# Performance work log

Measured on AMD Instinct MI355X. Metric: run time of the kernel, lower is better.

## Reference

```python
import jax, jax.numpy as jnp
import numpy as np

NUM_HEADS = 16
NEG_BIG = -1.0e9


def setup_inputs() -> dict:
    key = jax.random.key(0)
    k1, k2, k3 = jax.random.split(key, 3)
    B, S, D = 2, 2048, 1024
    x = jax.random.normal(k1, (B, S, D), dtype=jnp.float32)
    qkv_weights = jax.random.normal(k2, (D, 3 * D), dtype=jnp.float32) * (1.0 / np.sqrt(D))
    output_weights = jax.random.normal(k3, (D, D), dtype=jnp.float32) * (1.0 / np.sqrt(D))
    return {"x": x, "qkv_weights": qkv_weights, "output_weights": output_weights}


def reference(x, qkv_weights, output_weights):
    B, S, D = x.shape
    H = NUM_HEADS
    hd = D // H
    qkv = jnp.einsum('bsd,de->bse', x, qkv_weights)  # [B,S,3D]
    q, k, v = jnp.split(qkv, 3, axis=-1)
    # [B,H,S,hd]
    q = q.reshape(B, S, H, hd).transpose(0, 2, 1, 3)
    k = k.reshape(B, S, H, hd).transpose(0, 2, 1, 3)
    v = v.reshape(B, S, H, hd).transpose(0, 2, 1, 3)
    scores = jnp.einsum('bhqd,bhkd->bhqk', q, k)  # unscaled, matches original masked path
    # original bug: when masked, softmax is applied to UNSCALED scores with mask
    tril = jnp.tril(jnp.ones((S, S), dtype=scores.dtype))
    masked = scores * tril + NEG_BIG * (1.0 - tril)
    attn = jax.nn.softmax(masked, axis=-1)
    heads = jnp.einsum('bhqk,bhkd->bhqd', attn, v)  # [B,H,S,hd]
    merged = heads.transpose(0, 2, 1, 3).reshape(B, S, D)
    return jnp.einsum('bsd,de->bse', merged, output_weights)
```

## Files before the change

kernel.cpp:

```cpp
#include <hip/hip_runtime.h>
#include <stdint.h>

using u16 = unsigned short;
typedef __attribute__((ext_vector_type(8))) _Float16 half8;
typedef __attribute__((ext_vector_type(4))) float f32x4;
typedef __attribute__((ext_vector_type(4))) unsigned short u16x4;

#define S_LEN 2048
#define D_MODEL 1024
#define NHEAD 16
#define HDIM 64

__device__ __forceinline__ u16 f2h_bits(float f){
    _Float16 h = (_Float16)f;
    return __builtin_bit_cast(u16, h);
}
__device__ __forceinline__ float h2f_bits(u16 v){
    return (float)__builtin_bit_cast(_Float16, v);
}

typedef __attribute__((address_space(1))) void gvoid;
typedef __attribute__((address_space(3))) void lvoid;
__device__ __forceinline__ void gload_lds16(const u16* g, u16* l){
    __builtin_amdgcn_global_load_lds((gvoid*)(uintptr_t)g, (lvoid*)l, 16, 0, 0);
}

__device__ __constant__ signed char QB_T[40] = {3,7,7,10,11,11,11,14,14,15,15,15,15, 6,6,9,9,10,10,12,12,13,13,13,13,14,14, 2,5,5,8,8,8,9,12,12, 4,4, 1, 0};
__device__ __constant__ signed char LO_T[40] = {0,0,8,0,0,8,16,0,8,0,8,16,24, 0,7,0,7,8,15,0,7,0,7,14,21,16,23, 0,0,6,0,6,12,14,14,20, 0,5, 0, 0};
__device__ __constant__ signed char HI_T[40] = {8,8,16,8,8,16,24,8,16,8,16,24,32, 7,14,7,14,15,22,7,14,7,14,21,28,23,30, 6,6,12,6,12,18,20,20,26, 5,10, 4, 2};
__device__ __constant__ signed char PO_T[40] = {-1,6,7,14,17,18,19,28,29,32,33,34,35, 4,5,11,12,15,16,20,21,24,25,26,27,30,31, -1,2,3,8,9,10,13,22,23, 0,1, -1, -1};
__device__ __constant__ signed char NP_T[12] = {2,2,2,2,3,3,3,3,4,4,4,4};
__device__ __constant__ signed char OF_T[12] = {0,2,4,6,8,11,14,17,20,24,28,32};

__global__ __launch_bounds__(256) void k_cvt_x(const float* __restrict__ x, u16* __restrict__ xh){
    int i = blockIdx.x*256 + threadIdx.x;
    float4 v = reinterpret_cast<const float4*>(x)[i];
    u16x4 o;
    o.x = f2h_bits(v.x); o.y = f2h_bits(v.y); o.z = f2h_bits(v.z); o.w = f2h_bits(v.w);
    reinterpret_cast<u16x4*>(xh)[i] = o;
}

__global__ __launch_bounds__(256) void k_cvt_w(const float* __restrict__ W0, u16* __restrict__ T0,
                                               const float* __restrict__ W1, u16* __restrict__ T1){
    __shared__ float tt[32][33];
    int bx = blockIdx.x;
    const float* W; u16* WT; int N, n0;
    if (bx < 96){ W = W0; WT = T0; N = 3072; n0 = bx*32; }
    else        { W = W1; WT = T1; N = 1024; n0 = (bx-96)*32; }
    int k0 = blockIdx.y*32;
    int tx = threadIdx.x & 31, ty = threadIdx.x >> 5;
    #pragma unroll
    for (int i=0;i<4;++i) tt[ty+8*i][tx] = W[(size_t)(k0+ty+8*i)*N + n0+tx];
    __syncthreads();
    #pragma unroll
    for (int i=0;i<4;++i) WT[(size_t)(n0+ty+8*i)*1024 + k0+tx] = f2h_bits(tt[tx][ty+8*i]);
}

template<int EPI>
__global__ __launch_bounds__(256) void k_gemm(const u16* __restrict__ A, const u16* __restrict__ BT,
                                              float* __restrict__ Cf, u16* __restrict__ Qh,
                                              u16* __restrict__ Kh, u16* __restrict__ Vt){
    constexpr int Kd = 1024;
    __shared__ u16 As[2*128*32];
    __shared__ u16 Bs[2*128*32];
    int nwg = gridDim.x;
    int cpx = nwg >> 3;
    int wg  = ((int)blockIdx.x & 7)*cpx + ((int)blockIdx.x >> 3);
    int tm = wg & 31, tn = wg >> 5;
    int t = threadIdx.x;
    int w = t >> 6, lane = t & 63;
    int lr = lane & 15, lg = lane >> 4;
    int wm = (w>>1)*64, wn = (w&1)*64;
    int m0 = tm*128 + wm, n0 = tn*128 + wn;

    const u16* aG = A  + (size_t)(tm*128 + (t>>2))*Kd + (t&3)*8;
    const u16* bG = BT + (size_t)(tn*128 + (t>>2))*Kd + (t&3)*8;
    u16* aL = As + (t>>2)*32 + (t&3)*8;
    u16* bL = Bs + (t>>2)*32 + (t&3)*8;

    auto stage = [&](int buf, int kk){
        gload_lds16(aG + kk, aL + buf*4096);
        gload_lds16(aG + kk + (size_t)64*Kd, aL + buf*4096 + 64*32);
        gload_lds16(bG + kk, bL + buf*4096);
        gload_lds16(bG + kk + (size_t)64*Kd, bL + buf*4096 + 64*32);
    };

    f32x4 acc[4][4];
    #pragma unroll
    for (int i=0;i<4;++i)
        #pragma unroll
        for (int j=0;j<4;++j) acc[i][j] = (f32x4){0.f,0.f,0.f,0.f};

    stage(0, 0);
    __syncthreads();
    for (int kk=0; kk<Kd; kk+=32){
        int cur = (kk>>5) & 1;
        if (kk+32 < Kd) stage(cur^1, kk+32);

        half8 av[4], bv[4];
        #pragma unroll
        for (int mf=0;mf<4;++mf) av[mf] = *reinterpret_cast<const half8*>(&As[cur*4096 + (wm+mf*16+lr)*32 + lg*8]);
        #pragma unroll
        for (int nf=0;nf<4;++nf) bv[nf] = *reinterpret_cast<const half8*>(&Bs[cur*4096 + (wn+nf*16+lr)*32 + lg*8]);
        __builtin_amdgcn_s_setprio(1);
        #pragma unroll
        for (int mf=0;mf<4;++mf)
            #pragma unroll
            for (int nf=0;nf<4;++nf)
                acc[mf][nf] = __builtin_amdgcn_mfma_f32_16x16x32_f16(av[mf], bv[nf], acc[mf][nf], 0,0,0);
        __builtin_amdgcn_s_setprio(0);
        __syncthreads();
    }

    if (EPI == 0){
        #pragma unroll
        for (int mf=0;mf<4;++mf)
            #pragma unroll
            for (int nf=0;nf<4;++nf)
                #pragma unroll
                for (int j=0;j<4;++j)
                    Cf[(size_t)(m0+mf*16+lg*4+j)*D_MODEL + n0+nf*16+lr] = acc[mf][nf][j];
    } else {
        #pragma unroll
        for (int mf=0;mf<4;++mf){
            int r0 = m0 + mf*16 + lg*4;
            int b  = r0 >> 11, s = r0 & 2047;
            #pragma unroll
            for (int nf=0;nf<4;++nf){
                int col = n0 + nf*16 + lr;
                int which = col >> 10;
                int d  = col & 1023;
                int h  = d >> 6, di = d & 63;
                int bh = b*NHEAD + h;
                if (which == 2){
                    u16x4 pv;
                    pv.x = f2h_bits(acc[mf][nf][0]);
                    pv.y = f2h_bits(acc[mf][nf][1]);
                    pv.z = f2h_bits(acc[mf][nf][2]);
                    pv.w = f2h_bits(acc[mf][nf][3]);
                    *reinterpret_cast<u16x4*>(Vt + ((size_t)bh*HDIM + di)*S_LEN + s) = pv;
                } else {
                    u16* dst = (which==0 ? Qh : Kh) + ((size_t)bh*S_LEN + s)*HDIM + di;
                    #pragma unroll
                    for (int j=0;j<4;++j) dst[(size_t)j*HDIM] = f2h_bits(acc[mf][nf][j]);
                }
            }
        }
    }
}

__global__ __launch_bounds__(256,3) void k_attn(const u16* __restrict__ Q, const u16* __restrict__ K,
                                                const u16* __restrict__ Vt, u16* __restrict__ Mg,
                                                u16* __restrict__ On, float* __restrict__ Ml,
                                                float* __restrict__ Ll){
    __shared__ u16 Kl[2*64*64];
    __shared__ u16 Vl[2*64*64];
    __shared__ u16 plds[4][32][72];
    int t = threadIdx.x;
    int w = t >> 6, lane = t & 63;
    int lr = lane & 15, lg = lane >> 4;
    int blk = blockIdx.x;
    int bh  = blk & 31;
    int pi  = blk >> 5;
    int qb   = QB_T[pi];
    int ktLo = LO_T[pi];
    int ktHi = HI_T[pi];
    int po   = PO_T[pi];
    bool split = (po >= 0);
    int q0w = qb*128 + w*32;
    int b = bh >> 4, h = bh & 15;
    int pid = split ? bh*36 + po : 0;
    const u16* Qp = Q  + (size_t)bh*S_LEN*HDIM;
    const u16* Kp = K  + (size_t)bh*S_LEN*HDIM;
    const u16* Vp = Vt + (size_t)bh*HDIM*S_LEN;

    int c0 = t, c1 = t + 256;
    int r0 = c0 >> 3, s0 = 8*((c0 & 7) ^ (r0 & 7));
    int r1 = c1 >> 3, s1 = 8*((c1 & 7) ^ (r1 & 7));
    const u16* Ks0 = Kp + (size_t)r0*HDIM + s0;
    const u16* Ks1 = Kp + (size_t)r1*HDIM + s1;
    const u16* Vs0 = Vp + (size_t)r0*S_LEN + s0;
    const u16* Vs1 = Vp + (size_t)r1*S_LEN + s1;
    u16* Kd0 = Kl + c0*8; u16* Kd1 = Kl + c1*8;
    u16* Vd0 = Vl + c0*8; u16* Vd1 = Vl + c1*8;

    auto stageKV = [&](int buf, int kt){
        int kbase = kt*64;
        gload_lds16(Ks0 + (size_t)kbase*HDIM, Kd0 + buf*4096);
        gload_lds16(Ks1 + (size_t)kbase*HDIM, Kd1 + buf*4096);
        gload_lds16(Vs0 + kbase, Vd0 + buf*4096);
        gload_lds16(Vs1 + kbase, Vd1 + buf*4096);
    };

    half8 qf[2][2];
    #pragma unroll
    for (int qi=0;qi<2;++qi)
        #pragma unroll
        for (int ks=0;ks<2;++ks){
            half8 v = *reinterpret_cast<const half8*>(Qp + (size_t)(q0w+qi*16+lr)*HDIM + ks*32 + lg*8);
            #pragma unroll
            for (int j=0;j<8;++j) v[j] = v[j] * (_Float16)1.44269504f;
            qf[qi][ks] = v;
        }

    f32x4 oacc[2][4];
    float mrow[2], lrow[2];
    #pragma unroll
    for (int mf=0;mf<2;++mf){
        #pragma unroll
        for (int nf=0;nf<4;++nf) oacc[mf][nf] = (f32x4){0.f,0.f,0.f,0.f};
        mrow[mf] = -1e30f; lrow[mf] = 0.f;
    }

    int lastkt = (q0w + 31) >> 6;
    int swz = (lr & 7)*8;
    int nT = ktHi - ktLo;

    stageKV(0, ktLo);
    __syncthreads();
    for (int i=0; i<nT; ++i){
        int kt = ktLo + i;
        int cur = i & 1;
        if (i+1 < nT) stageKV(cur^1, kt+1);

        if (kt <= lastkt){
            const u16* Kb = Kl + cur*4096;
            const u16* Vb = Vl + cur*4096;
            int kbase = kt*64;
            half8 kfr[4][2];
            #pragma unroll
            for (int kf=0;kf<4;++kf)
                #pragma unroll
                for (int ks=0;ks<2;++ks)
                    kfr[kf][ks] = *reinterpret_cast<const half8*>(Kb + (kf*16+lr)*64 + ((ks*32 + lg*8) ^ swz));
            f32x4 sc[4][2];
            #pragma unroll
            for (int kf=0;kf<4;++kf)
                #pragma unroll
                for (int qi=0;qi<2;++qi) sc[kf][qi] = (f32x4){0.f,0.f,0.f,0.f};
            __builtin_amdgcn_s_setprio(1);
            #pragma unroll
            for (int kf=0;kf<4;++kf)
                #pragma unroll
                for (int qi=0;qi<2;++qi)
                    #pragma unroll
                    for (int ks=0;ks<2;++ks)
                        sc[kf][qi] = __builtin_amdgcn_mfma_f32_16x16x32_f16(kfr[kf][ks], qf[qi][ks], sc[kf][qi], 0,0,0);
            __builtin_amdgcn_s_setprio(0);

            half8 vf[4][2];
            #pragma unroll
            for (int nf=0;nf<4;++nf)
                #pragma unroll
                for (int kh=0;kh<2;++kh)
                    vf[nf][kh] = *reinterpret_cast<const half8*>(Vb + (nf*16+lr)*64 + ((kh*32 + lg*8) ^ swz));

            if (kt == lastkt){
                #pragma unroll
                for (int kf=0;kf<4;++kf)
                    #pragma unroll
                    for (int qi=0;qi<2;++qi)
                        #pragma unroll
                        for (int j=0;j<4;++j)
                            if (kbase+kf*16+lg*4+j > q0w+qi*16+lr) sc[kf][qi][j] = -1e9f;
            }

            float pmax[2];
            #pragma unroll
            for (int qi=0;qi<2;++qi){
                float t0 = fmaxf(fmaxf(sc[0][qi][0], sc[0][qi][1]), fmaxf(sc[0][qi][2], sc[0][qi][3]));
                float t1 = fmaxf(fmaxf(sc[1][qi][0], sc[1][qi][1]), fmaxf(sc[1][qi][2], sc[1][qi][3]));
                float t2 = fmaxf(fmaxf(sc[2][qi][0], sc[2][qi][1]), fmaxf(sc[2][qi][2], sc[2][qi][3]));
                float t3 = fmaxf(fmaxf(sc[3][qi][0], sc[3][qi][1]), fmaxf(sc[3][qi][2], sc[3][qi][3]));
                float tm = fmaxf(fmaxf(t0,t1), fmaxf(t2,t3));
                tm = fmaxf(tm, __shfl_xor(tm,16));
                tm = fmaxf(tm, __shfl_xor(tm,32));
                pmax[qi] = tm;
            }
            bool need = (pmax[0] > mrow[0]+8.0f) || (pmax[1] > mrow[1]+8.0f);
            if (__any(need)){
                float aq[2];
                #pragma unroll
                for (int qi=0;qi<2;++qi){
                    float mnew = fmaxf(mrow[qi], pmax[qi]);
                    aq[qi] = __builtin_amdgcn_exp2f(mrow[qi] - mnew);
                    mrow[qi] = mnew;
                    lrow[qi] *= aq[qi];
                }
                float am[2][4];
                #pragma unroll
                for (int mf=0;mf<2;++mf)
                    #pragma unroll
                    for (int j=0;j<4;++j) am[mf][j] = __shfl(aq[mf], lg*4+j);
                #pragma unroll
                for (int mf=0;mf<2;++mf)
                    #pragma unroll
                    for (int nf=0;nf<4;++nf)
                        #pragma unroll
                        for (int j=0;j<4;++j) oacc[mf][nf][j] *= am[mf][j];
            }
            #pragma unroll
            for (int qi=0;qi<2;++qi){
                float m = mrow[qi];
                float rs = 0.f;
                #pragma unroll
                for (int kf=0;kf<4;++kf)
                    #pragma unroll
                    for (int j=0;j<4;++j){
                        float e = __builtin_amdgcn_exp2f(sc[kf][qi][j] - m);
                        sc[kf][qi][j] = e;
                        rs += e;
                    }
                rs += __shfl_xor(rs,16);
                rs += __shfl_xor(rs,32);
                lrow[qi] += rs;
            }
            #pragma unroll
            for (int kf=0;kf<4;++kf)
                #pragma unroll
                for (int qi=0;qi<2;++qi){
                    u16x4 pk;
                    pk.x = f2h_bits(sc[kf][qi][0]);
                    pk.y = f2h_bits(sc[kf][qi][1]);
                    pk.z = f2h_bits(sc[kf][qi][2]);
                    pk.w = f2h_bits(sc[kf][qi][3]);
                    *reinterpret_cast<u16x4*>(&plds[w][qi*16+lr][kf*16+lg*4]) = pk;
                }
            half8 pa[2][2];
            #pragma unroll
            for (int mf=0;mf<2;++mf)
                #pragma unroll
                for (int kh=0;kh<2;++kh)
                    pa[mf][kh] = *reinterpret_cast<const half8*>(&plds[w][mf*16+lr][kh*32 + lg*8]);
            __builtin_amdgcn_s_setprio(1);
            #pragma unroll
            for (int mf=0;mf<2;++mf)
                #pragma unroll
                for (int nf=0;nf<4;++nf)
                    #pragma unroll
                    for (int kh=0;kh<2;++kh)
                        oacc[mf][nf] = __builtin_amdgcn_mfma_f32_16x16x32_f16(pa[mf][kh], vf[nf][kh], oacc[mf][nf], 0,0,0);
            __builtin_amdgcn_s_setprio(0);
        }
        __syncthreads();
    }

    float linv[2][4];
    #pragma unroll
    for (int mf=0;mf<2;++mf)
        #pragma unroll
        for (int j=0;j<4;++j) linv[mf][j] = 1.0f/__shfl(lrow[mf], lg*4+j);
    if (!split){
        #pragma unroll
        for (int mf=0;mf<2;++mf)
            #pragma unroll
            for (int nf=0;nf<4;++nf)
                #pragma unroll
                for (int j=0;j<4;++j)
                    Mg[(size_t)(b*S_LEN + q0w + mf*16 + lg*4 + j)*D_MODEL + h*HDIM + nf*16 + lr]
                        = f2h_bits(oacc[mf][nf][j]*linv[mf][j]);
    } else {
        #pragma unroll
        for (int mf=0;mf<2;++mf)
            #pragma unroll
            for (int nf=0;nf<4;++nf)
                #pragma unroll
                for (int j=0;j<4;++j)
                    On[(size_t)pid*8192 + (w*32 + mf*16 + lg*4 + j)*64 + nf*16 + lr]
                        = f2h_bits(oacc[mf][nf][j]*linv[mf][j]);
        if (lg == 0){
            #pragma unroll
            for (int qi=0;qi<2;++qi){
                Ml[pid*128 + w*32 + qi*16 + lr] = mrow[qi];
                Ll[pid*128 + w*32 + qi*16 + lr] = lrow[qi];
            }
        }
    }
}

__global__ __launch_bounds__(256) void k_comb(const u16* __restrict__ On, const float* __restrict__ Ml,
                                              const float* __restrict__ Ll, u16* __restrict__ Mg){
    int blk = blockIdx.x;
    int bh = blk & 31;
    int rest = blk >> 5;
    int qi = rest >> 3;
    int rq = rest & 7;
    int qb = 4 + qi;
    int np = NP_T[qi];
    int base = bh*36 + OF_T[qi];
    int b = bh >> 4, h = bh & 15;
    int t = threadIdx.x;
    int r  = rq*16 + (t >> 4);
    int cc = (t & 15) * 4;
    float osum0=0.f, osum1=0.f, osum2=0.f, osum3=0.f, wsum=0.f;
    float mm[4], ll[4];
    float M = -1e30f;
    #pragma unroll
    for (int p=0;p<4;++p){
        if (p < np){
            mm[p] = Ml[(base+p)*128 + r];
            ll[p] = Ll[(base+p)*128 + r];
            M = fmaxf(M, mm[p]);
        }
    }
    #pragma unroll
    for (int p=0;p<4;++p){
        if (p < np){
            float wgt = ll[p]*__builtin_amdgcn_exp2f(mm[p] - M);
            u16x4 ov = *reinterpret_cast<const u16x4*>(On + (size_t)(base+p)*8192 + r*64 + cc);
            osum0 += wgt*h2f_bits(ov[0]);
            osum1 += wgt*h2f_bits(ov[1]);
            osum2 += wgt*h2f_bits(ov[2]);
            osum3 += wgt*h2f_bits(ov[3]);
            wsum  += wgt;
        }
    }
    float inv = 1.0f/wsum;
    u16x4 o;
    o[0] = f2h_bits(osum0*inv);
    o[1] = f2h_bits(osum1*inv);
    o[2] = f2h_bits(osum2*inv);
    o[3] = f2h_bits(osum3*inv);
    *reinterpret_cast<u16x4*>(Mg + (size_t)(b*S_LEN + qb*128 + r)*D_MODEL + h*HDIM + cc) = o;
}

extern "C" void kernel_launch(void* const* d_in, const int* in_sizes, int n_in,
                              void* d_out, int out_size, void* d_ws, size_t ws_size,
                              hipStream_t stream) {
    const float* x    = (const float*)d_in[0];
    const float* wqkv = (const float*)d_in[1];
    const float* wout = (const float*)d_in[2];
    float* out = (float*)d_out;
    char* ws = (char*)d_ws;

    const size_t MB = 1u<<20;
    u16* xh     = (u16*)(ws + 0*MB);
    u16* wqkvT  = (u16*)(ws + 8*MB);
    u16* woutT  = (u16*)(ws + 14*MB);
    u16* Qh     = (u16*)(ws + 16*MB);
    u16* Kh     = (u16*)(ws + 24*MB);
    u16* Vt     = (u16*)(ws + 32*MB);
    u16* Mg     = (u16*)(ws + 40*MB);
    u16* On     = (u16*)(ws + 48*MB);
    float* Ml   = (float*)(ws + 67*MB);
    float* Ll   = (float*)(ws + 67*MB + 640*1024);

    k_cvt_x <<<4096, 256, 0, stream>>>(x, xh);
    k_cvt_w <<<dim3(128,32), 256, 0, stream>>>(wqkv, wqkvT, wout, woutT);
    k_gemm<1><<<768, 256, 0, stream>>>(xh, wqkvT, nullptr, Qh, Kh, Vt);
    k_attn  <<<1280, 256, 0, stream>>>(Qh, Kh, Vt, Mg, On, Ml, Ll);
    k_comb  <<<3072, 256, 0, stream>>>(On, Ml, Ll, Mg);
    k_gemm<0><<<256, 256, 0, stream>>>(Mg, woutT, out, nullptr, nullptr, nullptr);
}
```

Baseline: 118.2 us.

## Enlarge attention query tile to 256 rows with 8 waves and fuse conversion kernels

The attention kernel now processes 256 query rows per block with 512 threads (8 waves), so each staged K/V tile in LDS is shared by twice as many waves. The causal work-split tables, partial-output layout and combine kernel indexing are rebuilt for the coarser blocks. The x and weight conversion kernels are merged into a single launch. This removes one launch and halves K/V staging traffic per query row, but the coarser tiles give the causal schedule less load-balancing granularity and the larger blocks may lower occupancy.

```diff
diff --git a/kernel.cpp b/kernel.cpp
--- a/kernel.cpp
+++ b/kernel.cpp
@@ -25,29 +25,32 @@
     __builtin_amdgcn_global_load_lds((gvoid*)(uintptr_t)g, (lvoid*)l, 16, 0, 0);
 }
 
-__device__ __constant__ signed char QB_T[40] = {3,7,7,10,11,11,11,14,14,15,15,15,15, 6,6,9,9,10,10,12,12,13,13,13,13,14,14, 2,5,5,8,8,8,9,12,12, 4,4, 1, 0};
-__device__ __constant__ signed char LO_T[40] = {0,0,8,0,0,8,16,0,8,0,8,16,24, 0,7,0,7,8,15,0,7,0,7,14,21,16,23, 0,0,6,0,6,12,14,14,20, 0,5, 0, 0};
-__device__ __constant__ signed char HI_T[40] = {8,8,16,8,8,16,24,8,16,8,16,24,32, 7,14,7,14,15,22,7,14,7,14,21,28,23,30, 6,6,12,6,12,18,20,20,26, 5,10, 4, 2};
-__device__ __constant__ signed char PO_T[40] = {-1,6,7,14,17,18,19,28,29,32,33,34,35, 4,5,11,12,15,16,20,21,24,25,26,27,30,31, -1,2,3,8,9,10,13,22,23, 0,1, -1, -1};
-__device__ __constant__ signed char NP_T[12] = {2,2,2,2,3,3,3,3,4,4,4,4};
-__device__ __constant__ signed char OF_T[12] = {0,2,4,6,8,11,14,17,20,24,28,32};
-
-__global__ __launch_bounds__(256) void k_cvt_x(const float* __restrict__ x, u16* __restrict__ xh){
-    int i = blockIdx.x*256 + threadIdx.x;
-    float4 v = reinterpret_cast<const float4*>(x)[i];
-    u16x4 o;
-    o.x = f2h_bits(v.x); o.y = f2h_bits(v.y); o.z = f2h_bits(v.z); o.w = f2h_bits(v.w);
-    reinterpret_cast<u16x4*>(xh)[i] = o;
-}
-
-__global__ __launch_bounds__(256) void k_cvt_w(const float* __restrict__ W0, u16* __restrict__ T0,
-                                               const float* __restrict__ W1, u16* __restrict__ T1){
+__device__ __constant__ signed char QB_T[20] = {1,3,3,5,5,5,7,7,7,7, 4,4,6,6,6,6, 2,2,4, 0};
+__device__ __constant__ signed char LO_T[20] = {0,0,8,0,8,16,0,8,16,24, 0,7,0,7,14,21, 0,6,14, 0};
+__device__ __constant__ signed char HI_T[20] = {8,8,16,8,16,24,8,16,24,32, 7,14,7,14,21,28, 6,12,20, 4};
+__device__ __constant__ signed char PO_T[20] = {-1,2,3,7,8,9,14,15,16,17, 4,5,10,11,12,13, 0,1,6, -1};
+__device__ __constant__ signed char NP_T[6] = {2,2,3,3,4,4};
+__device__ __constant__ signed char OF_T[6] = {0,2,4,7,10,14};
+
+__global__ __launch_bounds__(256) void k_cvt(const float* __restrict__ x, u16* __restrict__ xh,
+                                             const float* __restrict__ W0, u16* __restrict__ T0,
+                                             const float* __restrict__ W1, u16* __restrict__ T1){
     __shared__ float tt[32][33];
-    int bx = blockIdx.x;
+    int blk = blockIdx.x;
+    if (blk < 4096){
+        int i = blk*256 + threadIdx.x;
+        float4 v = reinterpret_cast<const float4*>(x)[i];
+        u16x4 o;
+        o.x = f2h_bits(v.x); o.y = f2h_bits(v.y); o.z = f2h_bits(v.z); o.w = f2h_bits(v.w);
+        reinterpret_cast<u16x4*>(xh)[i] = o;
+        return;
+    }
+    int wi = blk - 4096;
+    int bx = wi & 127, ky = wi >> 7;
     const float* W; u16* WT; int N, n0;
     if (bx < 96){ W = W0; WT = T0; N = 3072; n0 = bx*32; }
     else        { W = W1; WT = T1; N = 1024; n0 = (bx-96)*32; }
-    int k0 = blockIdx.y*32;
+    int k0 = ky*32;
     int tx = threadIdx.x & 31, ty = threadIdx.x >> 5;
     #pragma unroll
     for (int i=0;i<4;++i) tt[ty+8*i][tx] = W[(size_t)(k0+ty+8*i)*N + n0+tx];
@@ -149,13 +152,13 @@
     }
 }
 
-__global__ __launch_bounds__(256,3) void k_attn(const u16* __restrict__ Q, const u16* __restrict__ K,
-                                                const u16* __restrict__ Vt, u16* __restrict__ Mg,
-                                                u16* __restrict__ On, float* __restrict__ Ml,
-                                                float* __restrict__ Ll){
+__global__ __launch_bounds__(512) void k_attn(const u16* __restrict__ Q, const u16* __restrict__ K,
+                                              const u16* __restrict__ Vt, u16* __restrict__ Mg,
+                                              u16* __restrict__ On, float* __restrict__ Ml,
+                                              float* __restrict__ Ll){
     __shared__ u16 Kl[2*64*64];
     __shared__ u16 Vl[2*64*64];
-    __shared__ u16 plds[4][32][72];
+    __shared__ u16 plds[8][32][72];
     int t = threadIdx.x;
     int w = t >> 6, lane = t & 63;
     int lr = lane & 15, lg = lane >> 4;
@@ -167,29 +170,23 @@
     int ktHi = HI_T[pi];
     int po   = PO_T[pi];
     bool split = (po >= 0);
-    int q0w = qb*128 + w*32;
+    int q0w = qb*256 + w*32;
     int b = bh >> 4, h = bh & 15;
-    int pid = split ? bh*36 + po : 0;
+    int pid = split ? bh*18 + po : 0;
     const u16* Qp = Q  + (size_t)bh*S_LEN*HDIM;
     const u16* Kp = K  + (size_t)bh*S_LEN*HDIM;
     const u16* Vp = Vt + (size_t)bh*HDIM*S_LEN;
 
-    int c0 = t, c1 = t + 256;
-    int r0 = c0 >> 3, s0 = 8*((c0 & 7) ^ (r0 & 7));
-    int r1 = c1 >> 3, s1 = 8*((c1 & 7) ^ (r1 & 7));
-    const u16* Ks0 = Kp + (size_t)r0*HDIM + s0;
-    const u16* Ks1 = Kp + (size_t)r1*HDIM + s1;
-    const u16* Vs0 = Vp + (size_t)r0*S_LEN + s0;
-    const u16* Vs1 = Vp + (size_t)r1*S_LEN + s1;
-    u16* Kd0 = Kl + c0*8; u16* Kd1 = Kl + c1*8;
-    u16* Vd0 = Vl + c0*8; u16* Vd1 = Vl + c1*8;
+    int r0 = t >> 3, s0 = 8*((t & 7) ^ (r0 & 7));
+    const u16* Ks = Kp + (size_t)r0*HDIM + s0;
+    const u16* Vs = Vp + (size_t)r0*S_LEN + s0;
+    u16* Kd = Kl + t*8;
+    u16* Vd = Vl + t*8;
 
     auto stageKV = [&](int buf, int kt){
         int kbase = kt*64;
-        gload_lds16(Ks0 + (size_t)kbase*HDIM, Kd0 + buf*4096);
-        gload_lds16(Ks1 + (size_t)kbase*HDIM, Kd1 + buf*4096);
-        gload_lds16(Vs0 + kbase, Vd0 + buf*4096);
-        gload_lds16(Vs1 + kbase, Vd1 + buf*4096);
+        gload_lds16(Ks + (size_t)kbase*HDIM, Kd + buf*4096);
+        gload_lds16(Vs + kbase, Vd + buf*4096);
     };
 
     half8 qf[2][2];
@@ -366,13 +363,13 @@
             for (int nf=0;nf<4;++nf)
                 #pragma unroll
                 for (int j=0;j<4;++j)
-                    On[(size_t)pid*8192 + (w*32 + mf*16 + lg*4 + j)*64 + nf*16 + lr]
+                    On[(size_t)pid*16384 + (w*32 + mf*16 + lg*4 + j)*64 + nf*16 + lr]
                         = f2h_bits(oacc[mf][nf][j]*linv[mf][j]);
         if (lg == 0){
             #pragma unroll
             for (int qi=0;qi<2;++qi){
-                Ml[pid*128 + w*32 + qi*16 + lr] = mrow[qi];
-                Ll[pid*128 + w*32 + qi*16 + lr] = lrow[qi];
+                Ml[pid*256 + w*32 + qi*16 + lr] = mrow[qi];
+                Ll[pid*256 + w*32 + qi*16 + lr] = lrow[qi];
             }
         }
     }
@@ -383,14 +380,14 @@
     int blk = blockIdx.x;
     int bh = blk & 31;
     int rest = blk >> 5;
-    int qi = rest >> 3;
-    int rq = rest & 7;
-    int qb = 4 + qi;
-    int np = NP_T[qi];
-    int base = bh*36 + OF_T[qi];
+    int qi6 = rest >> 4;
+    int rg = rest & 15;
+    int qb = 2 + qi6;
+    int np = NP_T[qi6];
+    int base = bh*18 + OF_T[qi6];
     int b = bh >> 4, h = bh & 15;
     int t = threadIdx.x;
-    int r  = rq*16 + (t >> 4);
+    int r  = rg*16 + (t >> 4);
     int cc = (t & 15) * 4;
     float osum0=0.f, osum1=0.f, osum2=0.f, osum3=0.f, wsum=0.f;
     float mm[4], ll[4];
@@ -398,8 +395,8 @@
     #pragma unroll
     for (int p=0;p<4;++p){
         if (p < np){
-            mm[p] = Ml[(base+p)*128 + r];
-            ll[p] = Ll[(base+p)*128 + r];
+            mm[p] = Ml[(base+p)*256 + r];
+            ll[p] = Ll[(base+p)*256 + r];
             M = fmaxf(M, mm[p]);
         }
     }
@@ -407,7 +404,7 @@
     for (int p=0;p<4;++p){
         if (p < np){
             float wgt = ll[p]*__builtin_amdgcn_exp2f(mm[p] - M);
-            u16x4 ov = *reinterpret_cast<const u16x4*>(On + (size_t)(base+p)*8192 + r*64 + cc);
+            u16x4 ov = *reinterpret_cast<const u16x4*>(On + (size_t)(base+p)*16384 + r*64 + cc);
             osum0 += wgt*h2f_bits(ov[0]);
             osum1 += wgt*h2f_bits(ov[1]);
             osum2 += wgt*h2f_bits(ov[2]);
@@ -421,7 +418,7 @@
     o[1] = f2h_bits(osum1*inv);
     o[2] = f2h_bits(osum2*inv);
     o[3] = f2h_bits(osum3*inv);
-    *reinterpret_cast<u16x4*>(Mg + (size_t)(b*S_LEN + qb*128 + r)*D_MODEL + h*HDIM + cc) = o;
+    *reinterpret_cast<u16x4*>(Mg + (size_t)(b*S_LEN + qb*256 + r)*D_MODEL + h*HDIM + cc) = o;
 }
 
 extern "C" void kernel_launch(void* const* d_in, const int* in_sizes, int n_in,
@@ -442,13 +439,12 @@
     u16* Vt     = (u16*)(ws + 32*MB);
     u16* Mg     = (u16*)(ws + 40*MB);
     u16* On     = (u16*)(ws + 48*MB);
-    float* Ml   = (float*)(ws + 67*MB);
-    float* Ll   = (float*)(ws + 67*MB + 640*1024);
-
-    k_cvt_x <<<4096, 256, 0, stream>>>(x, xh);
-    k_cvt_w <<<dim3(128,32), 256, 0, stream>>>(wqkv, wqkvT, wout, woutT);
+    float* Ml   = (float*)(ws + 66*MB);
+    float* Ll   = (float*)(ws + 66*MB + 640*1024);
+
+    k_cvt   <<<8192, 256, 0, stream>>>(x, xh, wqkv, wqkvT, wout, woutT);
     k_gemm<1><<<768, 256, 0, stream>>>(xh, wqkvT, nullptr, Qh, Kh, Vt);
-    k_attn  <<<1280, 256, 0, stream>>>(Qh, Kh, Vt, Mg, On, Ml, Ll);
+    k_attn  <<<640, 512, 0, stream>>>(Qh, Kh, Vt, Mg, On, Ml, Ll);
     k_comb  <<<3072, 256, 0, stream>>>(On, Ml, Ll, Mg);
     k_gemm<0><<<256, 256, 0, stream>>>(Mg, woutT, out, nullptr, nullptr, nullptr);
 }
```

After: 126.8 us. +7.3%, slower.
